# Kernel optimization log

Hardware: AMD Instinct MI355X
Metric: run time of the kernel (lower is better)

Reference implementation:

```python
import jax, jax.numpy as jnp
import numpy as np

B, L, H, V = 2048, 1024, 64, 64
LN_EPS = 1e-5
DELTA_EPS = 1e-6


def setup_inputs() -> dict:
    key = jax.random.key(0)
    ks = jax.random.split(key, 16)
    s = 0.05
    return {
        'seq': jax.random.randint(ks[0], (B, L), 0, V),
        'embed_W': jax.random.normal(ks[1], (V, H), jnp.float32),
        'ff_w1': jax.random.normal(ks[2], (H, 2 * H), jnp.float32) * s,
        'ff_b1': jnp.zeros((2 * H,), jnp.float32),
        'ff_w2': jax.random.normal(ks[3], (2 * H, H), jnp.float32) * s,
        'ff_b2': jnp.zeros((H,), jnp.float32),
        'ln_g': jnp.ones((H,), jnp.float32),
        'ln_b': jnp.zeros((H,), jnp.float32),
        'gate_w1': jax.random.normal(ks[4], (H, 16), jnp.float32) * s,
        'gate_b1': jnp.zeros((16,), jnp.float32),
        'gate_w2': jax.random.normal(ks[5], (16, 1), jnp.float32) * s,
        'gate_b2': jnp.zeros((1,), jnp.float32),
        'read_w': jax.random.normal(ks[6], (H, H), jnp.float32) * s,
        'read_b': jnp.zeros((H,), jnp.float32),
        'out_w': jax.random.normal(ks[7], (H, V), jnp.float32) * s,
        'out_b': jnp.zeros((V,), jnp.float32),
    }


def _layernorm(x, g, b):
    mu = jnp.mean(x, axis=-1, keepdims=True)
    var = jnp.var(x, axis=-1, keepdims=True)
    return (x - mu) * jax.lax.rsqrt(var + LN_EPS) * g + b


def reference(seq, embed_W, ff_w1, ff_b1, ff_w2, ff_b2, ln_g, ln_b,
              gate_w1, gate_b1, gate_w2, gate_b2, read_w, read_b, out_w, out_b):
    h = embed_W[seq]                                        # (B, L, H)
    ff = jnp.maximum(h @ ff_w1 + ff_b1, 0.0) @ ff_w2 + ff_b2
    h = _layernorm(h + ff, ln_g, ln_b)                      # (B, L, H)

    ks_seq = jnp.transpose(h[:, :-1, :], (1, 0, 2))         # (L-1, B, H) keys for scan

    def step(M, k):
        # k: (B, H); M: (B, H, H) fast-weight memory
        g = jax.nn.sigmoid(jnp.maximum(k @ gate_w1 + gate_b1, 0.0) @ gate_w2 + gate_b2)  # (B, 1)
        v_pred = jnp.einsum('bij,bj->bi', jax.lax.stop_gradient(M), k)
        denom = jnp.sum(k * k, axis=-1, keepdims=True) + DELTA_EPS
        dv = k - v_pred / denom                             # (B, H)
        dM = dv[:, :, None] * k[:, None, :]                 # outer product (B, H, H)
        return M + g[:, :, None] * dM, None

    M0 = jnp.zeros((h.shape[0], H, H), h.dtype)
    M, _ = jax.lax.scan(step, M0, ks_seq)

    q = h[:, -1, :]
    ctx = jnp.einsum('bij,bj->bi', M, q)                    # (B, H)
    logits = (ctx @ read_w + read_b) @ out_w + out_b        # (B, V)
    return logits
```

## Files before the change

### kernel.cpp

```cpp
#include <hip/hip_runtime.h>
#include <math.h>

#define Bsz 2048
#define Lsz 1024
#define SW  8

#define OFF_GC  0
#define OFF_PG  4160
#define OFF_H   8256
#define OFF_WC  12352
#define OFF_GV  16448
#define OFF_CI  16512
#define OFF_C   16576
#define OFF_BC  16640

__device__ __forceinline__ float __rlf(float v, int i) {
    return __int_as_float(__builtin_amdgcn_readlane(__float_as_int(v), i));
}

__global__ __launch_bounds__(128) void prep1_kernel(
    const float* __restrict__ embed_W, const float* __restrict__ ff_w1, const float* __restrict__ ff_b1,
    const float* __restrict__ ff_w2, const float* __restrict__ ff_b2, const float* __restrict__ ln_g,
    const float* __restrict__ ln_b, const float* __restrict__ gate_w1, const float* __restrict__ gate_b1,
    const float* __restrict__ gate_w2, const float* __restrict__ gate_b2, const float* __restrict__ read_w,
    const float* __restrict__ read_b, const float* __restrict__ out_w, const float* __restrict__ out_b,
    float* __restrict__ ws)
{
    const int tid = threadIdx.x;
    const int blk = blockIdx.x;
    if (blk < 64) {
        const int v = blk;
        __shared__ float z[128];
        __shared__ float hsh[64];
        const float* Ev = embed_W + (v << 6);
        float a = ff_b1[tid];
        #pragma unroll
        for (int i = 0; i < 64; ++i) a = fmaf(Ev[i], ff_w1[i * 128 + tid], a);
        z[tid] = fmaxf(a, 0.0f);
        __syncthreads();
        if (tid < 64) {
            float x = Ev[tid] + ff_b2[tid];
            #pragma unroll
            for (int j = 0; j < 128; ++j) x = fmaf(z[j], ff_w2[j * 64 + tid], x);
            float mu = x;
            #pragma unroll
            for (int off = 32; off > 0; off >>= 1) mu += __shfl_xor(mu, off);
            mu *= (1.0f / 64.0f);
            const float dd = x - mu;
            float var = dd * dd;
            #pragma unroll
            for (int off = 32; off > 0; off >>= 1) var += __shfl_xor(var, off);
            var *= (1.0f / 64.0f);
            const float rstd = rsqrtf(var + 1e-5f);
            const float hv = fmaf(dd * rstd, ln_g[tid], ln_b[tid]);
            hsh[tid] = hv;
            ws[OFF_H + (v << 6) + tid] = hv;
            float dn = hv * hv;
            #pragma unroll
            for (int off = 32; off > 0; off >>= 1) dn += __shfl_xor(dn, off);
            dn += 1e-6f;
            float a2 = 0.0f;
            if (tid < 16) {
                float um = gate_b1[tid];
                #pragma unroll
                for (int i = 0; i < 64; ++i) um = fmaf(hsh[i], gate_w1[i * 16 + tid], um);
                a2 = fmaxf(um, 0.0f) * gate_w2[tid];
            }
            #pragma unroll
            for (int off = 8; off > 0; off >>= 1) a2 += __shfl_xor(a2, off);
            if (tid == 0) {
                a2 += gate_b2[0];
                const float g = 1.0f / (1.0f + expf(-a2));
                ws[OFF_GV + v] = g;
                ws[OFF_C  + v] = g / dn;
                ws[OFF_CI + v] = dn / g;
            }
        }
    } else if (blk < 128) {
        const int j = blk - 64;
        if (tid < 64) {
            float a = 0.0f;
            #pragma unroll
            for (int m = 0; m < 64; ++m) a = fmaf(read_w[(j << 6) + m], out_w[(m << 6) + tid], a);
            ws[OFF_WC + (j << 6) + tid] = a;
        }
    } else {
        if (tid < 64) {
            float a = out_b[tid];
            #pragma unroll
            for (int jj = 0; jj < 64; ++jj) a = fmaf(read_b[jj], out_w[(jj << 6) + tid], a);
            ws[OFF_BC + tid] = a;
        }
    }
}

__global__ __launch_bounds__(64) void prep2_kernel(float* __restrict__ ws)
{
    const int tid = threadIdx.x;
    const int blk = blockIdx.x;
    if (blk == 128) { ws[OFF_GC + 64 * 64 + tid] = 0.0f; return; }
    __shared__ float tT[65 * 64];
    for (int idx = tid; idx < 4096; idx += 64) {
        const int w = idx >> 6, j = idx & 63;
        tT[j * 65 + w] = ws[OFF_H + idx];
    }
    __syncthreads();
    if (blk < 64) {
        const int v = blk;
        const float cv = ws[OFF_C + v];
        float a = 0.0f;
        #pragma unroll
        for (int j = 0; j < 64; ++j) a = fmaf(tT[j * 65 + v], tT[j * 65 + tid], a);
        ws[OFF_GC + (v << 6) + tid] = cv * a;
    } else {
        const int v = blk - 64;
        const float gv = ws[OFF_GV + v];
        float a = 0.0f;
        #pragma unroll
        for (int j = 0; j < 64; ++j)
            a = fmaf(tT[j * 65 + v], ws[OFF_WC + (j << 6) + tid], a);
        ws[OFF_PG + (v << 6) + tid] = gv * a;
    }
}

__global__ __launch_bounds__(SW * 64) void scan_kernel(const int* __restrict__ seq,
                                                       const float* __restrict__ ws,
                                                       float* __restrict__ out)
{
    __shared__ float ldsGc[65 * 64];
    __shared__ float ldsPg[64 * 64];

    const int tid  = threadIdx.x;
    const int wave = tid >> 6;
    const int lane = tid & 63;
    const int b    = blockIdx.x * SW + wave;

    const int4* ts = (const int4*)(seq + (size_t)b * Lsz);
    const int4 q0 = ts[lane], q1 = ts[64 + lane], q2 = ts[128 + lane], q3 = ts[192 + lane];

    {
        const float4* s1 = (const float4*)(ws + OFF_GC);
        float4* d1 = (float4*)ldsGc;
        for (int i = tid; i < 1040; i += SW * 64) d1[i] = s1[i];
        const float4* s2 = (const float4*)(ws + OFF_PG);
        float4* d2 = (float4*)ldsPg;
        for (int i = tid; i < 1024; i += SW * 64) d2[i] = s2[i];
    }

    int tv0 = q0.x | (q0.y << 8) | (q0.z << 16) | (q0.w << 24);
    int tv1 = q1.x | (q1.y << 8) | (q1.z << 16) | (q1.w << 24);
    int tv2 = q2.x | (q2.y << 8) | (q2.z << 16) | (q2.w << 24);
    int tv3 = q3.x | (q3.y << 8) | (q3.z << 16) | (q3.w << 24);

    const int tokL = (__builtin_amdgcn_readlane(tv3, 63) >> 24) & 0x7F;
    if (lane == 63) tv3 = (tv3 & 0x00FFFFFF) | (64 << 24);

    __syncthreads();

    float D = ldsGc[(tokL << 6) + lane] * ws[OFF_CI + tokL];
    float u = 0.0f;

    int   tk1[8], tk0[8], nk1[8], nk0[8];
    float gA[8], gB[8];

    auto EXT = [&](int wh, int wl, int* tk) {
        tk[0] = (wh >> 24) & 0x7F; tk[1] = (wh >> 16) & 0x7F;
        tk[2] = (wh >>  8) & 0x7F; tk[3] =  wh        & 0x7F;
        tk[4] = (wl >> 24) & 0x7F; tk[5] = (wl >> 16) & 0x7F;
        tk[6] = (wl >>  8) & 0x7F; tk[7] =  wl        & 0x7F;
    };
    auto ISSUE = [&](const int* tk, float* g) {
        #pragma unroll
        for (int k = 0; k < 8; ++k) g[k] = ldsGc[(tk[k] << 6) + lane];
    };
    auto STEP = [&](const int* tk, const float* g) {
        #pragma unroll
        for (int k = 0; k < 8; ++k) {
            const float d = __rlf(D, tk[k]);
            u += (lane == tk[k]) ? d : 0.0f;
            D = fmaf(-d, g[k], D);
        }
    };

    EXT(__builtin_amdgcn_readlane(tv3, 63), __builtin_amdgcn_readlane(tv3, 62), tk1);
    EXT(__builtin_amdgcn_readlane(tv3, 61), __builtin_amdgcn_readlane(tv3, 60), tk0);
    ISSUE(tk1, gA);

    #pragma unroll
    for (int p = 3; p >= 0; --p) {
        const int tvp = (p == 3) ? tv3 : (p == 2) ? tv2 : (p == 1) ? tv1 : tv0;
        for (int uu = 15; uu >= 1; --uu) {
            ISSUE(tk0, gB);
            STEP(tk1, gA);
            EXT(__builtin_amdgcn_readlane(tvp, 4 * uu - 1),
                __builtin_amdgcn_readlane(tvp, 4 * uu - 2), nk1);
            EXT(__builtin_amdgcn_readlane(tvp, 4 * uu - 3),
                __builtin_amdgcn_readlane(tvp, 4 * uu - 4), nk0);
            ISSUE(nk1, gA);
            STEP(tk0, gB);
            #pragma unroll
            for (int k = 0; k < 8; ++k) { tk1[k] = nk1[k]; tk0[k] = nk0[k]; }
        }
        ISSUE(tk0, gB);
        STEP(tk1, gA);
        if (p > 0) {
            const int tvn = (p == 3) ? tv2 : (p == 2) ? tv1 : tv0;
            EXT(__builtin_amdgcn_readlane(tvn, 63), __builtin_amdgcn_readlane(tvn, 62), nk1);
            EXT(__builtin_amdgcn_readlane(tvn, 61), __builtin_amdgcn_readlane(tvn, 60), nk0);
            ISSUE(nk1, gA);
            STEP(tk0, gB);
            #pragma unroll
            for (int k = 0; k < 8; ++k) { tk1[k] = nk1[k]; tk0[k] = nk0[k]; }
        } else {
            STEP(tk0, gB);
        }
    }

    float acc = ws[OFF_BC + lane];
    #pragma unroll 16
    for (int v = 0; v < 64; ++v)
        acc = fmaf(__rlf(u, v), ldsPg[(v << 6) + lane], acc);
    out[(size_t)b * 64 + lane] = acc;
}

extern "C" void kernel_launch(void* const* d_in, const int* in_sizes, int n_in,
                              void* d_out, int out_size, void* d_ws, size_t ws_size,
                              hipStream_t stream) {
    const int*   seq     = (const int*)  d_in[0];
    const float* embed_W = (const float*)d_in[1];
    const float* ff_w1   = (const float*)d_in[2];
    const float* ff_b1   = (const float*)d_in[3];
    const float* ff_w2   = (const float*)d_in[4];
    const float* ff_b2   = (const float*)d_in[5];
    const float* ln_g    = (const float*)d_in[6];
    const float* ln_b    = (const float*)d_in[7];
    const float* gate_w1 = (const float*)d_in[8];
    const float* gate_b1 = (const float*)d_in[9];
    const float* gate_w2 = (const float*)d_in[10];
    const float* gate_b2 = (const float*)d_in[11];
    const float* read_w  = (const float*)d_in[12];
    const float* read_b  = (const float*)d_in[13];
    const float* out_w   = (const float*)d_in[14];
    const float* out_b   = (const float*)d_in[15];
    float* ws  = (float*)d_ws;
    float* out = (float*)d_out;

    hipLaunchKernelGGL(prep1_kernel, dim3(129), dim3(128), 0, stream,
                       embed_W, ff_w1, ff_b1, ff_w2, ff_b2, ln_g, ln_b,
                       gate_w1, gate_b1, gate_w2, gate_b2, read_w, read_b,
                       out_w, out_b, ws);
    hipLaunchKernelGGL(prep2_kernel, dim3(129), dim3(64), 0, stream, ws);
    hipLaunchKernelGGL(scan_kernel, dim3(Bsz / SW), dim3(SW * 64), 0, stream,
                       seq, ws, out);
}
```

Baseline: 136.9 us.

## Hold per-lane Gram table in registers instead of gathering from LDS

Each lane now loads its 64-entry row of the scaled Gram table into two 32-wide register vectors. The per-token coefficient is picked by a wave-uniform dynamic register index plus a select, instead of an LDS gather. This removes the large LDS table, the double-buffered token extraction and prefetch pipeline, and the sentinel-token trick. prep2 is regrouped into 4-wave blocks and stores the table transposed with its scale applied per column. The cost is 64 extra VGPRs per lane and register-indexing instructions on the serial D dependency chain.

```diff
diff --git a/kernel.cpp b/kernel.cpp
--- a/kernel.cpp
+++ b/kernel.cpp
@@ -5,14 +5,16 @@
 #define Lsz 1024
 #define SW  8
 
-#define OFF_GC  0
-#define OFF_PG  4160
-#define OFF_H   8256
-#define OFF_WC  12352
-#define OFF_GV  16448
-#define OFF_CI  16512
-#define OFF_C   16576
-#define OFF_BC  16640
+#define OFF_GS  0
+#define OFF_PG  4096
+#define OFF_H   8192
+#define OFF_WC  12288
+#define OFF_GV  16384
+#define OFF_CI  16448
+#define OFF_C   16512
+#define OFF_BC  16576
+
+typedef float v32f __attribute__((ext_vector_type(32)));
 
 __device__ __forceinline__ float __rlf(float v, int i) {
     return __int_as_float(__builtin_amdgcn_readlane(__float_as_int(v), i));
@@ -94,32 +96,32 @@
     }
 }
 
-__global__ __launch_bounds__(64) void prep2_kernel(float* __restrict__ ws)
+__global__ __launch_bounds__(256) void prep2_kernel(float* __restrict__ ws)
 {
     const int tid = threadIdx.x;
     const int blk = blockIdx.x;
-    if (blk == 128) { ws[OFF_GC + 64 * 64 + tid] = 0.0f; return; }
     __shared__ float tT[65 * 64];
-    for (int idx = tid; idx < 4096; idx += 64) {
+    for (int idx = tid; idx < 4096; idx += 256) {
         const int w = idx >> 6, j = idx & 63;
         tT[j * 65 + w] = ws[OFF_H + idx];
     }
     __syncthreads();
-    if (blk < 64) {
-        const int v = blk;
-        const float cv = ws[OFF_C + v];
+    const int wave = tid >> 6, lane = tid & 63;
+    const int r = blk * 4 + wave;
+    if (r < 64) {
+        const int v = r;
         float a = 0.0f;
         #pragma unroll
-        for (int j = 0; j < 64; ++j) a = fmaf(tT[j * 65 + v], tT[j * 65 + tid], a);
-        ws[OFF_GC + (v << 6) + tid] = cv * a;
+        for (int j = 0; j < 64; ++j) a = fmaf(tT[j * 65 + v], tT[j * 65 + lane], a);
+        ws[OFF_GS + (v << 6) + lane] = ws[OFF_C + lane] * a;
     } else {
-        const int v = blk - 64;
+        const int v = r - 64;
         const float gv = ws[OFF_GV + v];
         float a = 0.0f;
         #pragma unroll
         for (int j = 0; j < 64; ++j)
-            a = fmaf(tT[j * 65 + v], ws[OFF_WC + (j << 6) + tid], a);
-        ws[OFF_PG + (v << 6) + tid] = gv * a;
+            a = fmaf(tT[j * 65 + v], ws[OFF_WC + (j << 6) + lane], a);
+        ws[OFF_PG + (v << 6) + lane] = gv * a;
     }
 }
 
@@ -127,8 +129,7 @@
                                                        const float* __restrict__ ws,
                                                        float* __restrict__ out)
 {
-    __shared__ float ldsGc[65 * 64];
-    __shared__ float ldsPg[64 * 64];
+    __shared__ float ldsPg[4096];
 
     const int tid  = threadIdx.x;
     const int wave = tid >> 6;
@@ -139,84 +140,64 @@
     const int4 q0 = ts[lane], q1 = ts[64 + lane], q2 = ts[128 + lane], q3 = ts[192 + lane];
 
     {
-        const float4* s1 = (const float4*)(ws + OFF_GC);
-        float4* d1 = (float4*)ldsGc;
-        for (int i = tid; i < 1040; i += SW * 64) d1[i] = s1[i];
         const float4* s2 = (const float4*)(ws + OFF_PG);
         float4* d2 = (float4*)ldsPg;
         for (int i = tid; i < 1024; i += SW * 64) d2[i] = s2[i];
     }
+
+    const v32f lo = *(const v32f*)(ws + OFF_GS + (lane << 6));
+    const v32f hi = *(const v32f*)(ws + OFF_GS + (lane << 6) + 32);
+    const float civ = ws[OFF_CI + lane];
+    const float bc  = ws[OFF_BC + lane];
 
     int tv0 = q0.x | (q0.y << 8) | (q0.z << 16) | (q0.w << 24);
     int tv1 = q1.x | (q1.y << 8) | (q1.z << 16) | (q1.w << 24);
     int tv2 = q2.x | (q2.y << 8) | (q2.z << 16) | (q2.w << 24);
     int tv3 = q3.x | (q3.y << 8) | (q3.z << 16) | (q3.w << 24);
 
-    const int tokL = (__builtin_amdgcn_readlane(tv3, 63) >> 24) & 0x7F;
-    if (lane == 63) tv3 = (tv3 & 0x00FFFFFF) | (64 << 24);
-
-    __syncthreads();
-
-    float D = ldsGc[(tokL << 6) + lane] * ws[OFF_CI + tokL];
+    const int tokL = (__builtin_amdgcn_readlane(tv3, 63) >> 24) & 0xFF;
+
+    float D;
+    {
+        const int t5 = tokL & 31;
+        const float a = lo[t5], h2 = hi[t5];
+        const float gs = (tokL & 32) ? h2 : a;
+        D = gs * __rlf(civ, tokL);
+    }
     float u = 0.0f;
 
-    int   tk1[8], tk0[8], nk1[8], nk0[8];
-    float gA[8], gB[8];
-
-    auto EXT = [&](int wh, int wl, int* tk) {
-        tk[0] = (wh >> 24) & 0x7F; tk[1] = (wh >> 16) & 0x7F;
-        tk[2] = (wh >>  8) & 0x7F; tk[3] =  wh        & 0x7F;
-        tk[4] = (wl >> 24) & 0x7F; tk[5] = (wl >> 16) & 0x7F;
-        tk[6] = (wl >>  8) & 0x7F; tk[7] =  wl        & 0x7F;
+    auto DO_STEP = [&](int tok) {
+        const int t5 = tok & 31;
+        const float a  = lo[t5];
+        const float h2 = hi[t5];
+        const float gc = (tok & 32) ? h2 : a;
+        const float d  = __rlf(D, tok);
+        u += (lane == tok) ? d : 0.0f;
+        D = fmaf(-d, gc, D);
     };
-    auto ISSUE = [&](const int* tk, float* g) {
-        #pragma unroll
-        for (int k = 0; k < 8; ++k) g[k] = ldsGc[(tk[k] << 6) + lane];
-    };
-    auto STEP = [&](const int* tk, const float* g) {
-        #pragma unroll
-        for (int k = 0; k < 8; ++k) {
-            const float d = __rlf(D, tk[k]);
-            u += (lane == tk[k]) ? d : 0.0f;
-            D = fmaf(-d, g[k], D);
-        }
-    };
-
-    EXT(__builtin_amdgcn_readlane(tv3, 63), __builtin_amdgcn_readlane(tv3, 62), tk1);
-    EXT(__builtin_amdgcn_readlane(tv3, 61), __builtin_amdgcn_readlane(tv3, 60), tk0);
-    ISSUE(tk1, gA);
-
+
+    {
+        const int wv = __builtin_amdgcn_readlane(tv3, 63);
+        DO_STEP((wv >> 16) & 0xFF);
+        DO_STEP((wv >>  8) & 0xFF);
+        DO_STEP( wv        & 0xFF);
+    }
     #pragma unroll
     for (int p = 3; p >= 0; --p) {
         const int tvp = (p == 3) ? tv3 : (p == 2) ? tv2 : (p == 1) ? tv1 : tv0;
-        for (int uu = 15; uu >= 1; --uu) {
-            ISSUE(tk0, gB);
-            STEP(tk1, gA);
-            EXT(__builtin_amdgcn_readlane(tvp, 4 * uu - 1),
-                __builtin_amdgcn_readlane(tvp, 4 * uu - 2), nk1);
-            EXT(__builtin_amdgcn_readlane(tvp, 4 * uu - 3),
-                __builtin_amdgcn_readlane(tvp, 4 * uu - 4), nk0);
-            ISSUE(nk1, gA);
-            STEP(tk0, gB);
-            #pragma unroll
-            for (int k = 0; k < 8; ++k) { tk1[k] = nk1[k]; tk0[k] = nk0[k]; }
-        }
-        ISSUE(tk0, gB);
-        STEP(tk1, gA);
-        if (p > 0) {
-            const int tvn = (p == 3) ? tv2 : (p == 2) ? tv1 : tv0;
-            EXT(__builtin_amdgcn_readlane(tvn, 63), __builtin_amdgcn_readlane(tvn, 62), nk1);
-            EXT(__builtin_amdgcn_readlane(tvn, 61), __builtin_amdgcn_readlane(tvn, 60), nk0);
-            ISSUE(nk1, gA);
-            STEP(tk0, gB);
-            #pragma unroll
-            for (int k = 0; k < 8; ++k) { tk1[k] = nk1[k]; tk0[k] = nk0[k]; }
-        } else {
-            STEP(tk0, gB);
-        }
-    }
-
-    float acc = ws[OFF_BC + lane];
+        const int ustart = (p == 3) ? 62 : 63;
+        for (int uu = ustart; uu >= 0; --uu) {
+            const int wv = __builtin_amdgcn_readlane(tvp, uu);
+            DO_STEP((wv >> 24) & 0xFF);
+            DO_STEP((wv >> 16) & 0xFF);
+            DO_STEP((wv >>  8) & 0xFF);
+            DO_STEP( wv        & 0xFF);
+        }
+    }
+
+    __syncthreads();
+
+    float acc = bc;
     #pragma unroll 16
     for (int v = 0; v < 64; ++v)
         acc = fmaf(__rlf(u, v), ldsPg[(v << 6) + lane], acc);
@@ -249,7 +230,7 @@
                        embed_W, ff_w1, ff_b1, ff_w2, ff_b2, ln_g, ln_b,
                        gate_w1, gate_b1, gate_w2, gate_b2, read_w, read_b,
                        out_w, out_b, ws);
-    hipLaunchKernelGGL(prep2_kernel, dim3(129), dim3(64), 0, stream, ws);
+    hipLaunchKernelGGL(prep2_kernel, dim3(32), dim3(256), 0, stream, ws);
     hipLaunchKernelGGL(scan_kernel, dim3(Bsz / SW), dim3(SW * 64), 0, stream,
                        seq, ws, out);
 }
```

After: 160.4 us. 1.17x slower.
